# Kernel tuning notes

Hardware: AMD Instinct MI355X
Metric: run time of the kernel (lower is better)

Reference implementation:

```python
import jax, jax.numpy as jnp
import numpy as np

HIDDEN = 1024
N_HEADS = 16
HEAD_DIM = HIDDEN // N_HEADS


def setup_inputs() -> dict:
    key = jax.random.key(0)
    ks = jax.random.split(key, 7)
    b, l, m = 4, 1024, 1024
    q = jax.random.normal(ks[0], (b, l, HIDDEN), dtype=jnp.float32)
    k = jax.random.normal(ks[1], (b, m, HIDDEN), dtype=jnp.float32)
    v = jax.random.normal(ks[2], (b, m, HIDDEN), dtype=jnp.float32)
    s = 1.0 / np.sqrt(HIDDEN)
    w_q = jax.random.normal(ks[3], (HIDDEN, HIDDEN), dtype=jnp.float32) * s
    w_k = jax.random.normal(ks[4], (HIDDEN, HIDDEN), dtype=jnp.float32) * s
    w_v = jax.random.normal(ks[5], (HIDDEN, HIDDEN), dtype=jnp.float32) * s
    w_o = jax.random.normal(ks[6], (HIDDEN, HIDDEN), dtype=jnp.float32) * s
    return {"q": q, "k": k, "v": v, "w_q": w_q, "w_k": w_k, "w_v": w_v, "w_o": w_o}


def reference(q, k, v, w_q, w_k, w_v, w_o):
    b, l, _ = q.shape
    _, m, _ = k.shape
    # Linear (bias=False): y = x @ W^T
    qp = q @ w_q.T
    kp = k @ w_k.T
    vp = v @ w_v.T  # projected but unused downstream (faithful to original bug)
    # Faithful non-standard split: hidden -> (head_dim, n_heads)
    qh = qp.reshape(b, l, HEAD_DIM, N_HEADS)
    kh = kp.reshape(b, m, HEAD_DIM, N_HEADS)
    # attn over K, scaled, softmax over m (dim=2)
    scores = jnp.einsum('bldn,bmdn->blmn', qh, kh) / np.sqrt(HEAD_DIM)
    attn = jax.nn.softmax(scores, axis=2)
    # dropout is identity in eval mode
    # NOTE: original attends over K (not V) — reproduced faithfully
    x = jnp.einsum('blmn,bmdn->bldn', attn, kh)
    x = x.reshape(b, l, HIDDEN)  # 'b l d n -> b l (d n)'
    return x @ w_o.T
```

## Files before the change

kernel.cpp:

```cpp
#include <hip/hip_runtime.h>
#include <hip/hip_bf16.h>
#include <stdint.h>
#include <math.h>


typedef __bf16 bf16;
typedef __bf16 bf16x8 __attribute__((ext_vector_type(8)));
typedef float  f32x4  __attribute__((ext_vector_type(4)));

__device__ __forceinline__ void async_load16(const void* g, void* l) {
  __builtin_amdgcn_global_load_lds((__attribute__((address_space(1))) void*)g,
                                   (__attribute__((address_space(3))) void*)l,
                                   16, 0, 0);
}

__device__ __forceinline__ float load_canon(const void* src, int i, int fl) {
  float f = fl ? ((const float*)src)[i] : (float)((const bf16*)src)[i];
  return fminf(fmaxf(f, -1024.f), 1024.f);
}

__global__ void __launch_bounds__(256)
canon_all(const void* __restrict__ q_raw, const void* __restrict__ k_raw,
          const void* __restrict__ wq_raw, const void* __restrict__ wk_raw,
          const void* __restrict__ wo_raw,
          bf16* __restrict__ q_c, bf16* __restrict__ k_c,
          bf16* __restrict__ wq_c, bf16* __restrict__ wk_c,
          bf16* __restrict__ wo_p, int* __restrict__ flag) {
  __shared__ int smax[4];
  const int tid = threadIdx.x;
  {
    int e = (((const unsigned short*)q_raw)[tid] >> 7) & 0xFF;
#pragma unroll
    for (int off = 1; off <= 32; off <<= 1) {
      int o = __shfl_xor(e, off);
      e = o > e ? o : e;
    }
    if ((tid & 63) == 0) smax[tid >> 6] = e;
  }
  __syncthreads();
  int m01 = smax[0] > smax[1] ? smax[0] : smax[1];
  int m23 = smax[2] > smax[3] ? smax[2] : smax[3];
  const int fl = ((m01 > m23 ? m01 : m23) >= 140) ? 1 : 0;

  const int blk = blockIdx.x;
  if (blk == 0 && tid == 0) *flag = fl;

  if (blk < 4096) {
    const void* src = blk < 2048 ? q_raw : k_raw;
    bf16* dst = blk < 2048 ? q_c : k_c;
    int i = (blk & 2047) * 2048 + tid * 8;
    bf16x8 v;
#pragma unroll
    for (int j = 0; j < 8; ++j) v[j] = (bf16)load_canon(src, i + j, fl);
    *(bf16x8*)(dst + i) = v;
  } else if (blk < 5120) {
    const void* src = blk < 4608 ? wq_raw : wk_raw;
    bf16* dst = blk < 4608 ? wq_c : wk_c;
    int i = ((blk - 4096) & 511) * 2048 + tid * 8;
    bf16x8 v;
#pragma unroll
    for (int j = 0; j < 8; ++j) v[j] = (bf16)load_canon(src, i + j, fl);
    *(bf16x8*)(dst + i) = v;
  } else {
    int d0 = (blk - 5120) * 2048 + tid * 8;
    int o = d0 >> 10, kp0 = d0 & 1023;
    bf16x8 v;
#pragma unroll
    for (int j = 0; j < 8; ++j) {
      int kp = kp0 + j;
      int h = ((kp & 63) << 4) | (kp >> 6);
      v[j] = (bf16)load_canon(wo_raw, o * 1024 + h, fl);
    }
    *(bf16x8*)(wo_p + d0) = v;
  }
}

__global__ void __launch_bounds__(256, 2)
qk_gemm(const bf16* __restrict__ q_c, const bf16* __restrict__ wq_c,
        const bf16* __restrict__ k_c, const bf16* __restrict__ wk_c,
        bf16* __restrict__ qh, bf16* __restrict__ kh, bf16* __restrict__ khT,
        float cs) {
  __shared__ __attribute__((aligned(16))) char smem[64 * 1024];
  bf16* sA  = (bf16*)smem;
  bf16* sB  = (bf16*)(smem + 32 * 1024);
  bf16* epi = (bf16*)smem;

  const int z = blockIdx.z;
  const bf16* A = z ? k_c : q_c;
  const bf16* W = z ? wk_c : wq_c;
  const float scale = z ? 1.0f : cs;
  bf16* out0 = z ? kh : qh;

  const int tid  = threadIdx.x;
  const int lane = tid & 63;
  const int wave = tid >> 6;
  const int q4   = lane >> 4;
  const int c16  = lane & 15;
  const int wm   = wave >> 1;
  const int wn   = wave & 1;

  const int lin    = blockIdx.x + 8 * blockIdx.y;
  const int rowBlk = (lin & 31) * 128;
  const int colBlk = (lin >> 5) * 128;

  int ar[8], ag[8];
#pragma unroll
  for (int i = 0; i < 8; ++i) {
    int s = tid + 256 * i;
    ar[i] = s >> 4;
    ag[i] = (s & 15) ^ (ar[i] & 15);
  }
  const bf16* gA[8];
  const bf16* gB[8];
  bf16 *lA[8], *lB[8];
#pragma unroll
  for (int i = 0; i < 8; ++i) {
    gA[i] = A + (size_t)(rowBlk + ar[i]) * 1024 + ag[i] * 8;
    gB[i] = W + (size_t)(colBlk + ar[i]) * 1024 + ag[i] * 8;
    lA[i] = sA + (tid + 256 * i) * 8;
    lB[i] = sB + (tid + 256 * i) * 8;
  }

  f32x4 acc[4][4] = {};

  for (int kk = 0; kk < 1024; kk += 128) {
    __syncthreads();
#pragma unroll
    for (int i = 0; i < 8; ++i) async_load16(gA[i] + kk, lA[i]);
#pragma unroll
    for (int i = 0; i < 8; ++i) async_load16(gB[i] + kk, lB[i]);
    __builtin_amdgcn_s_waitcnt(0);
    __syncthreads();

#pragma unroll
    for (int ks = 0; ks < 4; ++ks) {
      bf16x8 af[4], bfr[4];
#pragma unroll
      for (int mt = 0; mt < 4; ++mt) {
        int row = wm * 64 + mt * 16 + c16;
        af[mt] = *(const bf16x8*)(sA + row * 128 +
                   (((ks * 4 + q4) ^ (row & 15)) * 8));
      }
#pragma unroll
      for (int nt = 0; nt < 4; ++nt) {
        int row = wn * 64 + nt * 16 + c16;
        bfr[nt] = *(const bf16x8*)(sB + row * 128 +
                   (((ks * 4 + q4) ^ (row & 15)) * 8));
      }
#pragma unroll
      for (int mt = 0; mt < 4; ++mt)
#pragma unroll
        for (int nt = 0; nt < 4; ++nt)
          acc[mt][nt] = __builtin_amdgcn_mfma_f32_16x16x32_bf16(
              af[mt], bfr[nt], acc[mt][nt], 0, 0, 0);
    }
  }

  __syncthreads();
#pragma unroll
  for (int mt = 0; mt < 4; ++mt)
#pragma unroll
    for (int nt = 0; nt < 4; ++nt)
#pragma unroll
      for (int r = 0; r < 4; ++r) {
        int m_t = wm * 64 + mt * 16 + q4 * 4 + r;
        int h_t = wn * 64 + nt * 16 + c16;
        epi[m_t * 134 + h_t] = (bf16)(acc[mt][nt][r] * scale);
      }
  __syncthreads();

  const int bb    = rowBlk >> 10;
  const int mbase = rowBlk & 1023;
  const int dg0   = colBlk >> 4;

  {
    int n = tid >> 4;
#pragma unroll
    for (int i = 0; i < 8; ++i) {
      int m_t = (tid & 15) + i * 16;
      bf16x8 v;
#pragma unroll
      for (int dt = 0; dt < 8; ++dt) v[dt] = epi[m_t * 134 + dt * 16 + n];
      *(bf16x8*)(out0 + ((size_t)(bb * 16 + n) * 1024 + mbase + m_t) * 64 + dg0) = v;
    }
  }
  if (z) {
    int h_t = tid >> 1, half = tid & 1;
    int n = h_t & 15, dt = h_t >> 4;
    size_t base = ((size_t)(bb * 16 + n) * 64 + dg0 + dt) * 1024 + mbase + half * 64;
#pragma unroll
    for (int c = 0; c < 8; ++c) {
      bf16x8 v;
#pragma unroll
      for (int j = 0; j < 8; ++j) v[j] = epi[(half * 64 + c * 8 + j) * 134 + h_t];
      *(bf16x8*)(khT + base + c * 8) = v;
    }
  }
}

__global__ void __launch_bounds__(256, 2)
o_gemm(const bf16* __restrict__ A, const bf16* __restrict__ W,
       bf16* __restrict__ out0, float* __restrict__ outf,
       const int* __restrict__ flag) {
  __shared__ bf16 sA[128 * 128];
  __shared__ bf16 sB[64 * 128];

  const int tid  = threadIdx.x;
  const int lane = tid & 63;
  const int wave = tid >> 6;
  const int q4   = lane >> 4;
  const int c16  = lane & 15;
  const int wm   = wave >> 1;
  const int wn   = wave & 1;

  const int lin    = blockIdx.x + 16 * blockIdx.y;
  const int rowBlk = (lin & 31) * 128;
  const int colBlk = (lin >> 5) * 64;

  int ar[8], ag[8];
#pragma unroll
  for (int i = 0; i < 8; ++i) {
    int s = tid + 256 * i;
    ar[i] = s >> 4;
    ag[i] = (s & 15) ^ (ar[i] & 15);
  }
  const bf16* gA[8];
  bf16* lA[8];
#pragma unroll
  for (int i = 0; i < 8; ++i) {
    gA[i] = A + (size_t)(rowBlk + ar[i]) * 1024 + ag[i] * 8;
    lA[i] = sA + (tid + 256 * i) * 8;
  }
  const bf16* gB[4];
  bf16* lB[4];
#pragma unroll
  for (int i = 0; i < 4; ++i) {
    int s = tid + 256 * i;
    int br = s >> 4, bg = (s & 15) ^ (br & 15);
    gB[i] = W + (size_t)(colBlk + br) * 1024 + bg * 8;
    lB[i] = sB + s * 8;
  }

  f32x4 acc[4][2] = {};

  for (int kk = 0; kk < 1024; kk += 128) {
    __syncthreads();
#pragma unroll
    for (int i = 0; i < 8; ++i) async_load16(gA[i] + kk, lA[i]);
#pragma unroll
    for (int i = 0; i < 4; ++i) async_load16(gB[i] + kk, lB[i]);
    __builtin_amdgcn_s_waitcnt(0);
    __syncthreads();

#pragma unroll
    for (int ks = 0; ks < 4; ++ks) {
      bf16x8 af[4], bfr[2];
#pragma unroll
      for (int mt = 0; mt < 4; ++mt) {
        int row = wm * 64 + mt * 16 + c16;
        af[mt] = *(const bf16x8*)(sA + row * 128 +
                   (((ks * 4 + q4) ^ (row & 15)) * 8));
      }
#pragma unroll
      for (int nt = 0; nt < 2; ++nt) {
        int row = wn * 32 + nt * 16 + c16;
        bfr[nt] = *(const bf16x8*)(sB + row * 128 +
                   (((ks * 4 + q4) ^ (row & 15)) * 8));
      }
#pragma unroll
      for (int mt = 0; mt < 4; ++mt)
#pragma unroll
        for (int nt = 0; nt < 2; ++nt)
          acc[mt][nt] = __builtin_amdgcn_mfma_f32_16x16x32_bf16(
              af[mt], bfr[nt], acc[mt][nt], 0, 0, 0);
    }
  }

  const int fl = *flag;
#pragma unroll
  for (int mt = 0; mt < 4; ++mt)
#pragma unroll
    for (int nt = 0; nt < 2; ++nt)
#pragma unroll
      for (int r = 0; r < 4; ++r) {
        int gm = rowBlk + wm * 64 + mt * 16 + q4 * 4 + r;
        int gn = colBlk + wn * 32 + nt * 16 + c16;
        size_t idx = (size_t)gm * 1024 + gn;
        if (fl) outf[idx] = acc[mt][nt][r];
        else    out0[idx] = (bf16)acc[mt][nt][r];
      }
}

__global__ void __launch_bounds__(256, 2)
attn_kernel(const bf16* __restrict__ qh, const bf16* __restrict__ kh,
            const bf16* __restrict__ khT, bf16* __restrict__ xh) {
  __shared__ bf16 sK[128 * 64];
  __shared__ bf16 sKT[64 * 128];
  __shared__ bf16 sP[4][32 * 136];

  const int tid  = threadIdx.x;
  const int lane = tid & 63;
  const int wave = tid >> 6;
  const int q4   = lane >> 4;
  const int c16  = lane & 15;
  const int bn   = blockIdx.x;
  const int b    = bn >> 4, n = bn & 15;
  const int l0w  = blockIdx.y * 128 + wave * 32;

  const bf16* qhead  = qh  + (size_t)bn * (1024 * 64);
  const bf16* khead  = kh  + (size_t)bn * (1024 * 64);
  const bf16* kThead = khT + (size_t)bn * (64 * 1024);

  bf16x8 aq[2][2];
#pragma unroll
  for (int g = 0; g < 2; ++g)
#pragma unroll
    for (int hh = 0; hh < 2; ++hh)
      aq[g][hh] = *(const bf16x8*)(qhead +
                    (size_t)(l0w + g * 16 + c16) * 64 + hh * 32 + q4 * 8);

  int kr[4], kg[4], tr[4], tg[4];
#pragma unroll
  for (int i = 0; i < 4; ++i) {
    int s = tid + 256 * i;
    kr[i] = s >> 3;  kg[i] = (s & 7) ^ (kr[i] & 7);
    tr[i] = s >> 4;  tg[i] = (s & 15) ^ (tr[i] & 15);
  }

  f32x4 O[2][4] = {};
  f32x4 Osum[2] = {};
  bf16x8 ones;
#pragma unroll
  for (int j = 0; j < 8; ++j) ones[j] = (bf16)1.0f;
  bf16* sPw = sP[wave];

  for (int m0 = 0; m0 < 1024; m0 += 128) {
    __syncthreads();
#pragma unroll
    for (int i = 0; i < 4; ++i) {
      async_load16(khead + (size_t)(m0 + kr[i]) * 64 + kg[i] * 8,
                   sK + (tid + 256 * i) * 8);
      async_load16(kThead + (size_t)tr[i] * 1024 + m0 + tg[i] * 8,
                   sKT + (tid + 256 * i) * 8);
    }
    __builtin_amdgcn_s_waitcnt(0);
    __syncthreads();

    f32x4 S[2][8] = {};
#pragma unroll
    for (int t = 0; t < 8; ++t) {
#pragma unroll
      for (int hh = 0; hh < 2; ++hh) {
        int row = t * 16 + c16;
        bf16x8 bk = *(const bf16x8*)(sK + row * 64 +
                                     (((hh * 4 + q4) ^ (row & 7)) * 8));
        S[0][t] = __builtin_amdgcn_mfma_f32_16x16x32_bf16(aq[0][hh], bk, S[0][t], 0, 0, 0);
        S[1][t] = __builtin_amdgcn_mfma_f32_16x16x32_bf16(aq[1][hh], bk, S[1][t], 0, 0, 0);
      }
    }

#pragma unroll
    for (int g = 0; g < 2; ++g)
#pragma unroll
      for (int t = 0; t < 8; ++t)
#pragma unroll
        for (int r = 0; r < 4; ++r) {
          float p = __builtin_amdgcn_exp2f(S[g][t][r]);
          sPw[(g * 16 + q4 * 4 + r) * 136 + t * 16 + c16] = (bf16)p;
        }

    bf16x8 ap[2][4];
#pragma unroll
    for (int g = 0; g < 2; ++g) {
#pragma unroll
      for (int kk2 = 0; kk2 < 4; ++kk2) {
        ap[g][kk2] = *(const bf16x8*)(sPw + (g * 16 + c16) * 136 +
                                      kk2 * 32 + q4 * 8);
        Osum[g] = __builtin_amdgcn_mfma_f32_16x16x32_bf16(ap[g][kk2], ones, Osum[g], 0, 0, 0);
      }
    }

#pragma unroll
    for (int td = 0; td < 4; ++td) {
#pragma unroll
      for (int kk2 = 0; kk2 < 4; ++kk2) {
        int row = td * 16 + c16;
        bf16x8 bkt = *(const bf16x8*)(sKT + row * 128 +
                                      (((kk2 * 4 + q4) ^ (row & 15)) * 8));
        O[0][td] = __builtin_amdgcn_mfma_f32_16x16x32_bf16(ap[0][kk2], bkt, O[0][td], 0, 0, 0);
        O[1][td] = __builtin_amdgcn_mfma_f32_16x16x32_bf16(ap[1][kk2], bkt, O[1][td], 0, 0, 0);
      }
    }
  }

#pragma unroll
  for (int g = 0; g < 2; ++g) {
    float inv[4];
#pragma unroll
    for (int r = 0; r < 4; ++r) inv[r] = 1.0f / Osum[g][r];
#pragma unroll
    for (int td = 0; td < 4; ++td)
#pragma unroll
      for (int r = 0; r < 4; ++r)
        sPw[(g * 16 + q4 * 4 + r) * 136 + td * 16 + c16] = (bf16)(O[g][td][r] * inv[r]);
  }
  {
    int l_loc = lane >> 2, dq = lane & 3;
#pragma unroll
    for (int g = 0; g < 2; ++g) {
      bf16x8 v0 = *(const bf16x8*)(sPw + (g * 16 + l_loc) * 136 + dq * 16);
      bf16x8 v1 = *(const bf16x8*)(sPw + (g * 16 + l_loc) * 136 + dq * 16 + 8);
      size_t base = ((size_t)(b * 1024 + l0w + g * 16 + l_loc) * 16 + n) * 64 + dq * 16;
      *(bf16x8*)(xh + base)     = v0;
      *(bf16x8*)(xh + base + 8) = v1;
    }
  }
}

extern "C" void kernel_launch(void* const* d_in, const int* in_sizes, int n_in,
                              void* d_out, int out_size, void* d_ws, size_t ws_size,
                              hipStream_t stream) {
  const void* q_raw  = d_in[0];
  const void* k_raw  = d_in[1];
  const void* wq_raw = d_in[3];
  const void* wk_raw = d_in[4];
  const void* wo_raw = d_in[6];

  char* ws = (char*)d_ws;
  const size_t MB = 1024 * 1024;
  bf16* q_c  = (bf16*)(ws + 0 * MB);
  bf16* xh   = (bf16*)(ws + 0 * MB);
  bf16* k_c  = (bf16*)(ws + 8 * MB);
  bf16* kh   = (bf16*)(ws + 16 * MB);
  bf16* wq_c = (bf16*)(ws + 24 * MB);
  bf16* wk_c = (bf16*)(ws + 26 * MB);
  bf16* wo_p = (bf16*)(ws + 28 * MB);
  int*  flag = (int*)(ws + 30 * MB);
  bf16* qh   = (bf16*)d_out;
  bf16* khT  = (bf16*)((char*)d_out + 8 * MB);

  const float CS = 0.125f * 1.4426950408889634f;
  dim3 blk(256, 1, 1);

  hipLaunchKernelGGL(canon_all, dim3(5632), blk, 0, stream,
                     q_raw, k_raw, wq_raw, wk_raw, wo_raw,
                     q_c, k_c, wq_c, wk_c, wo_p, flag);
  hipLaunchKernelGGL(qk_gemm, dim3(8, 32, 2), blk, 0, stream,
                     q_c, wq_c, k_c, wk_c, qh, kh, khT, CS);
  hipLaunchKernelGGL(attn_kernel, dim3(64, 8, 1), blk, 0, stream,
                     qh, kh, khT, xh);
  hipLaunchKernelGGL(o_gemm, dim3(16, 32, 1), blk, 0, stream,
                     xh, wo_p, (bf16*)d_out, (float*)d_out, flag);
}
```

Before: 191.9 us.

## Fuse fp32-to-bf16 input conversion into the QK projection GEMM loads

```diff
diff --git a/kernel.cpp b/kernel.cpp
--- a/kernel.cpp
+++ b/kernel.cpp
@@ -14,84 +14,62 @@
                                    16, 0, 0);
 }
 
-__device__ __forceinline__ float load_canon(const void* src, int i, int fl) {
-  float f = fl ? ((const float*)src)[i] : (float)((const bf16*)src)[i];
-  return fminf(fmaxf(f, -1024.f), 1024.f);
-}
-
-__global__ void __launch_bounds__(256)
-canon_all(const void* __restrict__ q_raw, const void* __restrict__ k_raw,
-          const void* __restrict__ wq_raw, const void* __restrict__ wk_raw,
-          const void* __restrict__ wo_raw,
-          bf16* __restrict__ q_c, bf16* __restrict__ k_c,
-          bf16* __restrict__ wq_c, bf16* __restrict__ wk_c,
-          bf16* __restrict__ wo_p, int* __restrict__ flag) {
-  __shared__ int smax[4];
-  const int tid = threadIdx.x;
-  {
-    int e = (((const unsigned short*)q_raw)[tid] >> 7) & 0xFF;
-#pragma unroll
-    for (int off = 1; off <= 32; off <<= 1) {
-      int o = __shfl_xor(e, off);
-      e = o > e ? o : e;
-    }
-    if ((tid & 63) == 0) smax[tid >> 6] = e;
-  }
+__device__ __forceinline__ int detect_fl(const void* samp, int tid, int* smax) {
+  int e = (((const unsigned short*)samp)[tid] >> 7) & 0xFF;
+#pragma unroll
+  for (int off = 1; off <= 32; off <<= 1) {
+    int o = __shfl_xor(e, off);
+    e = o > e ? o : e;
+  }
+  if ((tid & 63) == 0) smax[tid >> 6] = e;
   __syncthreads();
   int m01 = smax[0] > smax[1] ? smax[0] : smax[1];
   int m23 = smax[2] > smax[3] ? smax[2] : smax[3];
-  const int fl = ((m01 > m23 ? m01 : m23) >= 140) ? 1 : 0;
-
-  const int blk = blockIdx.x;
-  if (blk == 0 && tid == 0) *flag = fl;
-
-  if (blk < 4096) {
-    const void* src = blk < 2048 ? q_raw : k_raw;
-    bf16* dst = blk < 2048 ? q_c : k_c;
-    int i = (blk & 2047) * 2048 + tid * 8;
-    bf16x8 v;
-#pragma unroll
-    for (int j = 0; j < 8; ++j) v[j] = (bf16)load_canon(src, i + j, fl);
-    *(bf16x8*)(dst + i) = v;
-  } else if (blk < 5120) {
-    const void* src = blk < 4608 ? wq_raw : wk_raw;
-    bf16* dst = blk < 4608 ? wq_c : wk_c;
-    int i = ((blk - 4096) & 511) * 2048 + tid * 8;
-    bf16x8 v;
-#pragma unroll
-    for (int j = 0; j < 8; ++j) v[j] = (bf16)load_canon(src, i + j, fl);
-    *(bf16x8*)(dst + i) = v;
-  } else {
-    int d0 = (blk - 5120) * 2048 + tid * 8;
-    int o = d0 >> 10, kp0 = d0 & 1023;
-    bf16x8 v;
-#pragma unroll
-    for (int j = 0; j < 8; ++j) {
-      int kp = kp0 + j;
-      int h = ((kp & 63) << 4) | (kp >> 6);
-      v[j] = (bf16)load_canon(wo_raw, o * 1024 + h, fl);
-    }
-    *(bf16x8*)(wo_p + d0) = v;
-  }
+  return ((m01 > m23 ? m01 : m23) >= 140) ? 1 : 0;
+}
+
+__global__ void __launch_bounds__(256)
+canon_wo(const void* __restrict__ wo_raw, bf16* __restrict__ wo_p,
+         int* __restrict__ flag) {
+  __shared__ int smax[4];
+  const int tid = threadIdx.x;
+  const int fl = detect_fl(wo_raw, tid, smax);
+  if (blockIdx.x == 0 && tid == 0) *flag = fl;
+
+  int d0 = blockIdx.x * 2048 + tid * 8;
+  int o = d0 >> 10, kp0 = d0 & 1023;
+  bf16x8 v;
+#pragma unroll
+  for (int j = 0; j < 8; ++j) {
+    int kp = kp0 + j;
+    int h = ((kp & 63) << 4) | (kp >> 6);
+    float f = fl ? ((const float*)wo_raw)[o * 1024 + h]
+                 : (float)((const bf16*)wo_raw)[o * 1024 + h];
+    f = fminf(fmaxf(f, -1024.f), 1024.f);
+    v[j] = (bf16)f;
+  }
+  *(bf16x8*)(wo_p + d0) = v;
 }
 
 __global__ void __launch_bounds__(256, 2)
-qk_gemm(const bf16* __restrict__ q_c, const bf16* __restrict__ wq_c,
-        const bf16* __restrict__ k_c, const bf16* __restrict__ wk_c,
+qk_gemm(const void* __restrict__ q_raw, const void* __restrict__ wq_raw,
+        const void* __restrict__ k_raw, const void* __restrict__ wk_raw,
         bf16* __restrict__ qh, bf16* __restrict__ kh, bf16* __restrict__ khT,
         float cs) {
-  __shared__ __attribute__((aligned(16))) char smem[64 * 1024];
-  bf16* sA  = (bf16*)smem;
-  bf16* sB  = (bf16*)(smem + 32 * 1024);
-  bf16* epi = (bf16*)smem;
+  __shared__ bf16 sA[128 * 64];
+  __shared__ bf16 sB[128 * 64];
+  __shared__ bf16 epi[128 * 134];
+  __shared__ int smax[4];
+
+  const int tid = threadIdx.x;
+  const int fl  = detect_fl(q_raw, tid, smax);
 
   const int z = blockIdx.z;
-  const bf16* A = z ? k_c : q_c;
-  const bf16* W = z ? wk_c : wq_c;
+  const void* A = z ? k_raw : q_raw;
+  const void* W = z ? wk_raw : wq_raw;
   const float scale = z ? 1.0f : cs;
   bf16* out0 = z ? kh : qh;
 
-  const int tid  = threadIdx.x;
   const int lane = tid & 63;
   const int wave = tid >> 6;
   const int q4   = lane >> 4;
@@ -103,57 +81,82 @@
   const int rowBlk = (lin & 31) * 128;
   const int colBlk = (lin >> 5) * 128;
 
-  int ar[8], ag[8];
-#pragma unroll
-  for (int i = 0; i < 8; ++i) {
+  int sr[4], sg[4];
+#pragma unroll
+  for (int i = 0; i < 4; ++i) {
     int s = tid + 256 * i;
-    ar[i] = s >> 4;
-    ag[i] = (s & 15) ^ (ar[i] & 15);
-  }
-  const bf16* gA[8];
-  const bf16* gB[8];
-  bf16 *lA[8], *lB[8];
-#pragma unroll
-  for (int i = 0; i < 8; ++i) {
-    gA[i] = A + (size_t)(rowBlk + ar[i]) * 1024 + ag[i] * 8;
-    gB[i] = W + (size_t)(colBlk + ar[i]) * 1024 + ag[i] * 8;
-    lA[i] = sA + (tid + 256 * i) * 8;
-    lB[i] = sB + (tid + 256 * i) * 8;
+    sr[i] = s >> 3;
+    sg[i] = (s & 7) ^ (sr[i] & 7);
   }
 
   f32x4 acc[4][4] = {};
 
-  for (int kk = 0; kk < 1024; kk += 128) {
-    __syncthreads();
-#pragma unroll
-    for (int i = 0; i < 8; ++i) async_load16(gA[i] + kk, lA[i]);
-#pragma unroll
-    for (int i = 0; i < 8; ++i) async_load16(gB[i] + kk, lB[i]);
-    __builtin_amdgcn_s_waitcnt(0);
-    __syncthreads();
-
-#pragma unroll
-    for (int ks = 0; ks < 4; ++ks) {
-      bf16x8 af[4], bfr[4];
+  for (int kk = 0; kk < 1024; kk += 64) {
+    __syncthreads();
+    {
+      bf16x8 st[4];
+      if (fl) {
+#pragma unroll
+        for (int i = 0; i < 4; ++i) {
+          const float* p = (const float*)A +
+              (size_t)(rowBlk + sr[i]) * 1024 + kk + sg[i] * 8;
+#pragma unroll
+          for (int j = 0; j < 8; ++j) st[i][j] = (bf16)p[j];
+        }
+      } else {
+#pragma unroll
+        for (int i = 0; i < 4; ++i)
+          st[i] = *(const bf16x8*)((const bf16*)A +
+              (size_t)(rowBlk + sr[i]) * 1024 + kk + sg[i] * 8);
+      }
+#pragma unroll
+      for (int i = 0; i < 4; ++i) *(bf16x8*)(sA + (tid + 256 * i) * 8) = st[i];
+    }
+    {
+      bf16x8 st[4];
+      if (fl) {
+#pragma unroll
+        for (int i = 0; i < 4; ++i) {
+          const float* p = (const float*)W +
+              (size_t)(colBlk + sr[i]) * 1024 + kk + sg[i] * 8;
+#pragma unroll
+          for (int j = 0; j < 8; ++j) st[i][j] = (bf16)p[j];
+        }
+      } else {
+#pragma unroll
+        for (int i = 0; i < 4; ++i)
+          st[i] = *(const bf16x8*)((const bf16*)W +
+              (size_t)(colBlk + sr[i]) * 1024 + kk + sg[i] * 8);
+      }
+#pragma unroll
+      for (int i = 0; i < 4; ++i) *(bf16x8*)(sB + (tid + 256 * i) * 8) = st[i];
+    }
+    __syncthreads();
+
+    bf16x8 af[2][4], bfr[2][4];
+#pragma unroll
+    for (int ks = 0; ks < 2; ++ks) {
 #pragma unroll
       for (int mt = 0; mt < 4; ++mt) {
         int row = wm * 64 + mt * 16 + c16;
-        af[mt] = *(const bf16x8*)(sA + row * 128 +
-                   (((ks * 4 + q4) ^ (row & 15)) * 8));
+        af[ks][mt] = *(const bf16x8*)(sA + row * 64 +
+                       (((ks * 4 + q4) ^ (row & 7)) * 8));
       }
 #pragma unroll
       for (int nt = 0; nt < 4; ++nt) {
         int row = wn * 64 + nt * 16 + c16;
-        bfr[nt] = *(const bf16x8*)(sB + row * 128 +
-                   (((ks * 4 + q4) ^ (row & 15)) * 8));
-      }
+        bfr[ks][nt] = *(const bf16x8*)(sB + row * 64 +
+                       (((ks * 4 + q4) ^ (row & 7)) * 8));
+      }
+    }
+#pragma unroll
+    for (int ks = 0; ks < 2; ++ks)
 #pragma unroll
       for (int mt = 0; mt < 4; ++mt)
 #pragma unroll
         for (int nt = 0; nt < 4; ++nt)
           acc[mt][nt] = __builtin_amdgcn_mfma_f32_16x16x32_bf16(
-              af[mt], bfr[nt], acc[mt][nt], 0, 0, 0);
-    }
+              af[ks][mt], bfr[ks][nt], acc[mt][nt], 0, 0, 0);
   }
 
   __syncthreads();
@@ -428,12 +431,8 @@
 
   char* ws = (char*)d_ws;
   const size_t MB = 1024 * 1024;
-  bf16* q_c  = (bf16*)(ws + 0 * MB);
   bf16* xh   = (bf16*)(ws + 0 * MB);
-  bf16* k_c  = (bf16*)(ws + 8 * MB);
   bf16* kh   = (bf16*)(ws + 16 * MB);
-  bf16* wq_c = (bf16*)(ws + 24 * MB);
-  bf16* wk_c = (bf16*)(ws + 26 * MB);
   bf16* wo_p = (bf16*)(ws + 28 * MB);
   int*  flag = (int*)(ws + 30 * MB);
   bf16* qh   = (bf16*)d_out;
@@ -442,11 +441,10 @@
   const float CS = 0.125f * 1.4426950408889634f;
   dim3 blk(256, 1, 1);
 
-  hipLaunchKernelGGL(canon_all, dim3(5632), blk, 0, stream,
-                     q_raw, k_raw, wq_raw, wk_raw, wo_raw,
-                     q_c, k_c, wq_c, wk_c, wo_p, flag);
+  hipLaunchKernelGGL(canon_wo, dim3(512), blk, 0, stream,
+                     wo_raw, wo_p, flag);
   hipLaunchKernelGGL(qk_gemm, dim3(8, 32, 2), blk, 0, stream,
-                     q_c, wq_c, k_c, wk_c, qh, kh, khT, CS);
+                     q_raw, wq_raw, k_raw, wk_raw, qh, kh, khT, CS);
   hipLaunchKernelGGL(attn_kernel, dim3(64, 8, 1), blk, 0, stream,
                      qh, kh, khT, xh);
   hipLaunchKernelGGL(o_gemm, dim3(16, 32, 1), blk, 0, stream,
```

Result: no change. 188.7 us (-1.7%).
